# Performance work log

Hardware: AMD Instinct MI355X
Metric: run time of the kernel (lower is better)

The kernel has to match this reference:

```python
import jax, jax.numpy as jnp
import numpy as np

B, C, H, W = 64, 128, 56, 56
ALPHA = 0.001


def _build_inhi_mat(out_channels):
    # Circulant 0/1 band: row i has ones at columns (i-r//2 ... i+r//2) mod C,
    # exactly matching the torch double loop with modular wrap-around.
    r = out_channels // 8 + 1  # inhiRange
    i = np.arange(out_channels)[:, None]
    d = np.arange(-(r // 2), r // 2 + 1)[None, :]
    cols = (i + d) % out_channels  # [C, r]
    m = np.zeros((out_channels, out_channels), dtype=np.float32)
    m[np.repeat(i, d.shape[1], axis=1), cols] = 1.0
    return m


def setup_inputs() -> dict:
    key = jax.random.key(0)
    x = jax.random.normal(key, (B, C, H, W), dtype=jnp.float32)
    inhiMat = jnp.asarray(_build_inhi_mat(C))  # [C, C] constant buffer
    return {"x": x, "inhiMat": inhiMat}


def reference(x, inhiMat):
    b, c, h, w = x.shape
    inhiRange = c // 8 + 1
    # y = detach(x)^2 -> banded cross-channel sum (bmm with broadcast [C,C] mat)
    y = jax.lax.stop_gradient(x) ** 2
    y = y.reshape(b, c, h * w)
    y = jnp.einsum('ij,bjs->bis', inhiMat, y)  # same math as bmm with tiled inhi
    y = y.reshape(b, c, h, w)
    denom = (y * ALPHA / inhiRange + 1.0) ** 0.75
    return x / denom
```

## Files before the change

kernel.cpp:

```cpp
#include <hip/hip_runtime.h>


#define B_DIM 64
#define C_DIM 128
#define HW_DIM (56 * 56)
#define HW4 (HW_DIM / 4)
#define NSEG 4
#define SEGC (C_DIM / NSEG)

__device__ __forceinline__ float pow_m075(float t) {
    return __builtin_amdgcn_exp2f(-0.75f * __builtin_amdgcn_logf(t));
}

__global__ __launch_bounds__(256) void lrn_kernel(const float4* __restrict__ x,
                                                  float4* __restrict__ out) {
    const float kAlphaOverR = 0.001f / 17.0f;

    const int col = blockIdx.x * blockDim.x + threadIdx.x;
    const int b   = col / HW4;
    const int hw4 = col - b * HW4;
    const int c0  = blockIdx.y * SEGC;

    const float4* base = x + ((size_t)b * C_DIM) * HW4 + hw4;
    float4* obase      = out + ((size_t)b * C_DIM) * HW4 + hw4;

    float4 s = make_float4(0.f, 0.f, 0.f, 0.f);
#pragma unroll
    for (int d = -8; d <= 8; ++d) {
        const int ch = (c0 + d + C_DIM) & (C_DIM - 1);
        const float4 v = base[(size_t)ch * HW4];
        s.x += v.x * v.x;
        s.y += v.y * v.y;
        s.z += v.z * v.z;
        s.w += v.w * v.w;
    }

#pragma unroll 8
    for (int i = 0; i < SEGC; ++i) {
        const int c = c0 + i;
        const float4 xc = base[(size_t)c * HW4];

        float4 r;
        r.x = xc.x * pow_m075(fmaf(s.x, kAlphaOverR, 1.0f));
        r.y = xc.y * pow_m075(fmaf(s.y, kAlphaOverR, 1.0f));
        r.z = xc.z * pow_m075(fmaf(s.z, kAlphaOverR, 1.0f));
        r.w = xc.w * pow_m075(fmaf(s.w, kAlphaOverR, 1.0f));
        obase[(size_t)c * HW4] = r;

        const int ci = (c + 9) & (C_DIM - 1);
        const int co = (c - 8 + C_DIM) & (C_DIM - 1);
        const float4 vin  = base[(size_t)ci * HW4];
        const float4 vout = base[(size_t)co * HW4];
        s.x += vin.x * vin.x - vout.x * vout.x;
        s.y += vin.y * vin.y - vout.y * vout.y;
        s.z += vin.z * vin.z - vout.z * vout.z;
        s.w += vin.w * vin.w - vout.w * vout.w;
    }
}

extern "C" void kernel_launch(void* const* d_in, const int* in_sizes, int n_in,
                              void* d_out, int out_size, void* d_ws, size_t ws_size,
                              hipStream_t stream) {
    const float4* x = (const float4*)d_in[0];
    float4* out = (float4*)d_out;

    dim3 grid(196, NSEG);
    lrn_kernel<<<grid, 256, 0, stream>>>(x, out);
}
```

Baseline: 209.3 us.

## Use float2 columns with full-channel sliding window per thread

Each thread now owns a float2 column and slides the 17-channel window across all 128 channels, replacing four channel segments per float4 column. This removes the redundant 16-channel warm-up reads each segment paid, so less traffic is re-read. It also launches 64-thread blocks over twice as many columns. In exchange, each thread's serial channel loop is four times longer and the loads are narrower, which may reduce memory-level parallelism per thread.

```diff
diff --git a/kernel.cpp b/kernel.cpp
--- a/kernel.cpp
+++ b/kernel.cpp
@@ -4,66 +4,56 @@
 #define B_DIM 64
 #define C_DIM 128
 #define HW_DIM (56 * 56)
-#define HW4 (HW_DIM / 4)
-#define NSEG 4
-#define SEGC (C_DIM / NSEG)
+#define HW2 (HW_DIM / 2)
+#define NCOL (B_DIM * HW2)
 
 __device__ __forceinline__ float pow_m075(float t) {
     return __builtin_amdgcn_exp2f(-0.75f * __builtin_amdgcn_logf(t));
 }
 
-__global__ __launch_bounds__(256) void lrn_kernel(const float4* __restrict__ x,
-                                                  float4* __restrict__ out) {
+__global__ __launch_bounds__(64) void lrn_kernel(const float2* __restrict__ x,
+                                                 float2* __restrict__ out) {
     const float kAlphaOverR = 0.001f / 17.0f;
 
-    const int col = blockIdx.x * blockDim.x + threadIdx.x;
-    const int b   = col / HW4;
-    const int hw4 = col - b * HW4;
-    const int c0  = blockIdx.y * SEGC;
+    const int col = blockIdx.x * 64 + threadIdx.x;
+    const int b   = col / HW2;
+    const int hw2 = col - b * HW2;
 
-    const float4* base = x + ((size_t)b * C_DIM) * HW4 + hw4;
-    float4* obase      = out + ((size_t)b * C_DIM) * HW4 + hw4;
+    const float2* base = x + ((size_t)b * C_DIM) * HW2 + hw2;
+    float2* obase      = out + ((size_t)b * C_DIM) * HW2 + hw2;
 
-    float4 s = make_float4(0.f, 0.f, 0.f, 0.f);
+    float sx = 0.f, sy = 0.f;
 #pragma unroll
     for (int d = -8; d <= 8; ++d) {
-        const int ch = (c0 + d + C_DIM) & (C_DIM - 1);
-        const float4 v = base[(size_t)ch * HW4];
-        s.x += v.x * v.x;
-        s.y += v.y * v.y;
-        s.z += v.z * v.z;
-        s.w += v.w * v.w;
+        const int ch = (d + C_DIM) & (C_DIM - 1);
+        const float2 v = base[(size_t)ch * HW2];
+        sx += v.x * v.x;
+        sy += v.y * v.y;
     }
 
 #pragma unroll 8
-    for (int i = 0; i < SEGC; ++i) {
-        const int c = c0 + i;
-        const float4 xc = base[(size_t)c * HW4];
+    for (int c = 0; c < C_DIM; ++c) {
+        const float2 xc = base[(size_t)c * HW2];
 
-        float4 r;
-        r.x = xc.x * pow_m075(fmaf(s.x, kAlphaOverR, 1.0f));
-        r.y = xc.y * pow_m075(fmaf(s.y, kAlphaOverR, 1.0f));
-        r.z = xc.z * pow_m075(fmaf(s.z, kAlphaOverR, 1.0f));
-        r.w = xc.w * pow_m075(fmaf(s.w, kAlphaOverR, 1.0f));
-        obase[(size_t)c * HW4] = r;
+        float2 r;
+        r.x = xc.x * pow_m075(fmaf(sx, kAlphaOverR, 1.0f));
+        r.y = xc.y * pow_m075(fmaf(sy, kAlphaOverR, 1.0f));
+        obase[(size_t)c * HW2] = r;
 
         const int ci = (c + 9) & (C_DIM - 1);
         const int co = (c - 8 + C_DIM) & (C_DIM - 1);
-        const float4 vin  = base[(size_t)ci * HW4];
-        const float4 vout = base[(size_t)co * HW4];
-        s.x += vin.x * vin.x - vout.x * vout.x;
-        s.y += vin.y * vin.y - vout.y * vout.y;
-        s.z += vin.z * vin.z - vout.z * vout.z;
-        s.w += vin.w * vin.w - vout.w * vout.w;
+        const float2 vin  = base[(size_t)ci * HW2];
+        const float2 vout = base[(size_t)co * HW2];
+        sx += vin.x * vin.x - vout.x * vout.x;
+        sy += vin.y * vin.y - vout.y * vout.y;
     }
 }
 
 extern "C" void kernel_launch(void* const* d_in, const int* in_sizes, int n_in,
                               void* d_out, int out_size, void* d_ws, size_t ws_size,
                               hipStream_t stream) {
-    const float4* x = (const float4*)d_in[0];
-    float4* out = (float4*)d_out;
+    const float2* x = (const float2*)d_in[0];
+    float2* out = (float2*)d_out;
 
-    dim3 grid(196, NSEG);
-    lrn_kernel<<<grid, 256, 0, stream>>>(x, out);
+    lrn_kernel<<<NCOL / 64, 64, 0, stream>>>(x, out);
 }
```

Measured after the change: 193.5 us. 1.08x faster.
